# Performance work log

Measured on AMD Instinct MI355X. Metric: run time of the kernel, lower is better.

The kernel has to match this reference:

```python
import jax, jax.numpy as jnp
import numpy as np

IMG_SIZE = 640
NUM_CLASSES = 80
KA = 3
STRIDES = (8, 16, 32)
CONF_THRESH = 0.001
NMS_THRESH = 0.6
ANCHORS = np.array([[12, 16], [19, 36], [40, 28],
                    [36, 75], [76, 55], [72, 146],
                    [142, 110], [192, 243], [459, 401]], np.float32).reshape(3, 3, 2)
CLS_OFFSET = 4.0  # > max normalized coord (1.0); separates classes for class-wise NMS


def _make_grid(stride):
    f = IMG_SIZE // stride
    gy, gx = jnp.meshgrid(jnp.arange(f), jnp.arange(f), indexing='ij')
    # [HW, 1, 2] in (x, y) order, row-major over (H, W) like permute(1,2,0).view(-1,...)
    return jnp.stack([gx, gy], axis=-1).reshape(-1, 1, 2).astype(jnp.float32)


def _decode_level(pred, level):
    # pred: [KA*(1+C+4), H, W] -> obj [HW*KA,1], cls [HW*KA,C], boxes [HW*KA,4]
    C = NUM_CLASSES
    p = jnp.transpose(pred, (1, 2, 0)).reshape(-1, KA * (1 + C + 4))  # [HW, ch]
    obj = p[:, :KA].reshape(-1, 1)
    cls = p[:, KA:KA * (1 + C)].reshape(-1, C)
    reg = p[:, KA * (1 + C):].reshape(-1, KA, 4)
    grid = _make_grid(STRIDES[level])               # [HW, 1, 2]
    anchors = jnp.asarray(ANCHORS[level])           # [KA, 2]
    xy = (jax.nn.sigmoid(reg[..., :2]) + grid) * STRIDES[level]
    wh = jnp.exp(reg[..., 2:]) * anchors
    box = jnp.concatenate([xy - wh * 0.5, xy + wh * 0.5], axis=-1).reshape(-1, 4)
    return obj, cls, box


def _greedy_nms(boxes, scores, valid, thresh):
    # Faithful sequential greedy NMS (same math as the numpy loop), via lax.scan.
    N = boxes.shape[0]
    order = jnp.argsort(-scores)
    b = boxes[order]
    v = valid[order]
    areas = (b[:, 2] - b[:, 0]) * (b[:, 3] - b[:, 1])
    idx = jnp.arange(N)

    def step(suppressed, i):
        keep_i = v[i] & jnp.logical_not(suppressed[i])
        xx1 = jnp.maximum(b[i, 0], b[:, 0])
        yy1 = jnp.maximum(b[i, 1], b[:, 1])
        xx2 = jnp.minimum(b[i, 2], b[:, 2])
        yy2 = jnp.minimum(b[i, 3], b[:, 3])
        w = jnp.maximum(1e-28, xx2 - xx1)
        h = jnp.maximum(1e-28, yy2 - yy1)
        inter = w * h
        ovr = inter / (areas[i] + areas - inter + 1e-14)
        suppressed = suppressed | (keep_i & (ovr > thresh) & (idx > i))
        return suppressed, keep_i

    _, kept_sorted = jax.lax.scan(step, jnp.zeros(N, bool), idx)
    return jnp.zeros(N, bool).at[order].set(kept_sorted)


def _forward(pred_s, pred_m, pred_l):
    outs = [_decode_level(p, i) for i, p in enumerate((pred_s, pred_m, pred_l))]
    obj = jnp.concatenate([o[0] for o in outs], axis=0)   # [N, 1]
    cls = jnp.concatenate([o[1] for o in outs], axis=0)   # [N, C]
    box = jnp.concatenate([o[2] for o in outs], axis=0)   # [N, 4]
    bboxes = jnp.clip(box / IMG_SIZE, 0.0, 1.0)
    scores = jax.nn.sigmoid(obj) * jax.nn.softmax(cls, axis=-1)  # [N, C]
    cls_inds = jnp.argmax(scores, axis=1)
    conf = jnp.max(scores, axis=1)
    valid = conf >= CONF_THRESH
    # per-class NMS == class-offset trick: different classes never overlap
    nms_boxes = bboxes + cls_inds.astype(bboxes.dtype)[:, None] * CLS_OFFSET
    keep = _greedy_nms(jax.lax.stop_gradient(nms_boxes),
                       jax.lax.stop_gradient(conf), valid, NMS_THRESH)
    return bboxes, conf, cls_inds, keep


def setup_inputs() -> dict:
    key = jax.random.key(0)
    k1, k2, k3 = jax.random.split(key, 3)
    ch = KA * (1 + NUM_CLASSES + 4)  # 255
    return {
        'pred_s': jax.random.normal(k1, (ch, 80, 80), jnp.float32),
        'pred_m': jax.random.normal(k2, (ch, 40, 40), jnp.float32),
        'pred_l': jax.random.normal(k3, (ch, 20, 20), jnp.float32),
    }


def reference(pred_s, pred_m, pred_l):
    # returns fixed-shape (bboxes [N,4], scores [N], cls_inds [N], keep mask [N])
    return _forward(pred_s, pred_m, pred_l)
```

## Files before the change

### kernel.cpp

```cpp
#include <hip/hip_runtime.h>

typedef unsigned long long u64;
typedef unsigned int u32;

#define N_TOT 25200
#define NCLS 80
#define CAP 512

__device__ __constant__ float c_AW[9] = {12.f,19.f,40.f,36.f,76.f,72.f,142.f,192.f,459.f};
__device__ __constant__ float c_AH[9] = {16.f,36.f,28.f,75.f,55.f,146.f,110.f,243.f,401.f};

__global__ __launch_bounds__(256)
void decode_kernel(const float* __restrict__ p0,
                   const float* __restrict__ p1,
                   const float* __restrict__ p2,
                   float* __restrict__ out)
{
    const int t = blockIdx.x * 256 + threadIdx.x;
    const int n = t >> 3;
    const int q = t & 7;
    if (n >= N_TOT) return;

    const float* p; int f, strd, base, lvl;
    if (n < 19200)      { p = p0; f = 80; strd = 8;  base = 0;     lvl = 0; }
    else if (n < 24000) { p = p1; f = 40; strd = 16; base = 19200; lvl = 1; }
    else                { p = p2; f = 20; strd = 32; base = 24000; lvl = 2; }

    const int r  = n - base;
    const int hw = r / 3;
    const int a  = r - hw * 3;
    const int HW = f * f;
    const int gx = hw % f;
    const int gy = hw / f;
    const float* cell = p + hw;
    const float* clsp = cell + (3 + a * NCLS) * HW;

    float obj = 0.f, tx = 0.f, ty = 0.f, tw = 0.f, th = 0.f;
    if (q == 0) {
        obj = cell[a * HW];
        const float* regp = cell + (243 + a * 4) * HW;
        tx = regp[0];
        ty = regp[HW];
        tw = regp[2 * HW];
        th = regp[3 * HW];
    }

    float v[10];
    #pragma unroll
    for (int k = 0; k < 10; ++k) v[k] = clsp[(8 * k + q) * HW];

    float lmax = v[0];
    #pragma unroll
    for (int k = 1; k < 10; ++k) lmax = fmaxf(lmax, v[k]);
    float gm = lmax;
    gm = fmaxf(gm, __shfl_xor(gm, 1));
    gm = fmaxf(gm, __shfl_xor(gm, 2));
    gm = fmaxf(gm, __shfl_xor(gm, 4));

    float ls = 0.f, bp = -1.f; int ba_ = 0;
    #pragma unroll
    for (int k = 0; k < 10; ++k) {
        float pc = expf(v[k] - gm);
        ls += pc;
        if (pc > bp) { bp = pc; ba_ = 8 * k + q; }
    }
    float gs = ls;
    gs += __shfl_xor(gs, 1);
    gs += __shfl_xor(gs, 2);
    gs += __shfl_xor(gs, 4);
    {
        float bp2; int ba2;
        bp2 = __shfl_xor(bp, 1); ba2 = __shfl_xor(ba_, 1);
        if (bp2 > bp || (bp2 == bp && ba2 < ba_)) { bp = bp2; ba_ = ba2; }
        bp2 = __shfl_xor(bp, 2); ba2 = __shfl_xor(ba_, 2);
        if (bp2 > bp || (bp2 == bp && ba2 < ba_)) { bp = bp2; ba_ = ba2; }
        bp2 = __shfl_xor(bp, 4); ba2 = __shfl_xor(ba_, 4);
        if (bp2 > bp || (bp2 == bp && ba2 < ba_)) { bp = bp2; ba_ = ba2; }
    }

    if (q != 0) return;

    float sig  = 1.f / (1.f + expf(-obj));
    float conf = sig * (bp / gs);

    float sx = 1.f / (1.f + expf(-tx));
    float sy = 1.f / (1.f + expf(-ty));
    float cx = (sx + (float)gx) * (float)strd;
    float cy = (sy + (float)gy) * (float)strd;
    const int ai = lvl * 3 + a;
    float w  = expf(tw) * c_AW[ai];
    float h  = expf(th) * c_AH[ai];
    float hx = w * 0.5f, hy = h * 0.5f;
    float x1 = (cx - hx) / 640.0f;
    float y1 = (cy - hy) / 640.0f;
    float x2 = (cx + hx) / 640.0f;
    float y2 = (cy + hy) / 640.0f;
    x1 = fminf(fmaxf(x1, 0.f), 1.f);
    y1 = fminf(fmaxf(y1, 0.f), 1.f);
    x2 = fminf(fmaxf(x2, 0.f), 1.f);
    y2 = fminf(fmaxf(y2, 0.f), 1.f);

    *(float4*)(out + n * 4) = make_float4(x1, y1, x2, y2);
    out[100800 + n] = conf;
    out[126000 + n] = (float)ba_;
    out[151200 + n] = 0.0f;
}

__global__ __launch_bounds__(1024)
void nms_kernel(const float* __restrict__ out,
                float* __restrict__ out_keep)
{
    const int c = blockIdx.x;
    const int tid = threadIdx.x;
    const int wave = tid >> 6, lane = tid & 63;

    __shared__ int    scnt;
    __shared__ u64    skey[CAP];
    __shared__ float4 sbox[CAP + 1];
    __shared__ int    sgi[CAP];
    __shared__ u64    maskT[8 * CAP];

    if (tid == 0) scnt = 0;
    __syncthreads();

    const float* confp = out + 100800;
    const float* clsp  = out + 126000;
    const u64 lt = (1ull << lane) - 1ull;
    for (int itr = 0; itr < 7; ++itr) {
        const int ib = itr * 1024 + tid;
        const bool inb = (ib < 6300);
        float4 cf4 = make_float4(-1.f, -1.f, -1.f, -1.f);
        float4 cl4 = make_float4(0.f, 0.f, 0.f, 0.f);
        if (inb) {
            cf4 = *(const float4*)(confp + ib * 4);
            cl4 = *(const float4*)(clsp  + ib * 4);
        }
        const bool m0 = inb && ((int)cl4.x == c) && (cf4.x >= 0.001f);
        const bool m1 = inb && ((int)cl4.y == c) && (cf4.y >= 0.001f);
        const bool m2 = inb && ((int)cl4.z == c) && (cf4.z >= 0.001f);
        const bool m3 = inb && ((int)cl4.w == c) && (cf4.w >= 0.001f);
        const u64 b0 = __ballot(m0), b1 = __ballot(m1), b2 = __ballot(m2), b3 = __ballot(m3);
        const int t0 = __popcll(b0), t1 = __popcll(b1), t2 = __popcll(b2), t3 = __popcll(b3);
        const int tot = t0 + t1 + t2 + t3;
        int base = 0;
        if (tot) {
            if (lane == 0) base = atomicAdd(&scnt, tot);
            base = __shfl(base, 0);
            const int i0 = itr * 4096 + tid * 4;
            int pos;
            if (m0) { pos = base + __popcll(b0 & lt);
                      if (pos < CAP) skey[pos] = ((u64)__float_as_uint(cf4.x) << 32) | (u64)(~(u32)(i0)); }
            if (m1) { pos = base + t0 + __popcll(b1 & lt);
                      if (pos < CAP) skey[pos] = ((u64)__float_as_uint(cf4.y) << 32) | (u64)(~(u32)(i0 + 1)); }
            if (m2) { pos = base + t0 + t1 + __popcll(b2 & lt);
                      if (pos < CAP) skey[pos] = ((u64)__float_as_uint(cf4.z) << 32) | (u64)(~(u32)(i0 + 2)); }
            if (m3) { pos = base + t0 + t1 + t2 + __popcll(b3 & lt);
                      if (pos < CAP) skey[pos] = ((u64)__float_as_uint(cf4.w) << 32) | (u64)(~(u32)(i0 + 3)); }
        }
    }
    __syncthreads();
    const int M  = min(scnt, CAP);
    const int MW = (M + 63) >> 6;

    if (wave < MW) {
        const int e = (wave << 6) + lane;
        if (e < M) {
            const u64 ke = skey[e];
            int rank = 0;
            int j = 0;
            for (; j + 8 <= M; j += 8) {
                rank += (int)(skey[j]   > ke) + (int)(skey[j+1] > ke)
                      + (int)(skey[j+2] > ke) + (int)(skey[j+3] > ke)
                      + (int)(skey[j+4] > ke) + (int)(skey[j+5] > ke)
                      + (int)(skey[j+6] > ke) + (int)(skey[j+7] > ke);
            }
            for (; j < M; ++j) rank += (int)(skey[j] > ke);

            const u32 gi = ~(u32)ke;
            const float4 b = *(const float4*)(out + gi * 4);
            const float off = 4.0f * (float)c;
            sbox[rank] = make_float4(b.x + off, b.y + off, b.z + off, b.w + off);
            sgi[rank]  = (int)gi;
        }
    }
    __syncthreads();

    const int ntiles = (MW * (MW + 1)) >> 1;
    for (int t = wave; t < ntiles; t += 16) {
        int rw = 0, acc = 0;
        while (t >= acc + (MW - rw)) { acc += MW - rw; ++rw; }
        const int cw = rw + (t - acc);
        const int j  = (cw << 6) + lane;
        const float4 cb = sbox[min(j, M - 1)];
        const float  ca = (cb.z - cb.x) * (cb.w - cb.y);
        const int r0 = rw << 6;
        const int r1 = min(r0 + 64, M);
        u64 bits = 0ull;
        float4 nb = sbox[r0];
        for (int i = r0; i < r1; ++i) {
            const float4 rb = nb;
            nb = sbox[i + 1];
            const float ra = (rb.z - rb.x) * (rb.w - rb.y);
            float xx1 = fmaxf(rb.x, cb.x);
            float yy1 = fmaxf(rb.y, cb.y);
            float xx2 = fminf(rb.z, cb.z);
            float yy2 = fminf(rb.w, cb.w);
            float ww = fmaxf(1e-28f, xx2 - xx1);
            float hh = fmaxf(1e-28f, yy2 - yy1);
            float inter = ww * hh;
            float ovr = inter / (ra + ca - inter + 1e-14f);
            bits |= (u64)((i < j) && (ovr >= 0.6f)) << (i & 63);
        }
        maskT[rw * CAP + j] = bits;
    }
    __syncthreads();

    if (wave != 0) return;

    u64 k0 = 0, k1 = 0, k2 = 0, k3 = 0, k4 = 0, k5 = 0, k6 = 0, k7 = 0;
    (void)k7;
#define MT(W) maskT[(W) * CAP + j]
#define TILE(W, PRE)                                                    \
    if ((W) < MW) {                                                     \
        const int j = ((W) << 6) + lane;                                \
        const u64 mine = MT(W);                                         \
        const u64 pre = (PRE);                                          \
        const int rm = M - ((W) << 6);                                  \
        const u64 valid = (rm >= 64) ? ~0ull : ((1ull << rm) - 1ull);   \
        u64 cand = valid & ~__ballot(pre != 0ull);                      \
        u64 kept = 0ull;                                                \
        while (cand) {                                                  \
            const u64 remv = cand & __ballot((mine & kept) != 0ull);    \
            cand &= ~remv;                                              \
            const u64 newk = cand & __ballot((mine & cand) == 0ull);    \
            kept |= newk;                                               \
            cand &= ~newk;                                              \
        }                                                               \
        k##W = kept;                                                    \
        if ((kept >> lane) & 1ull) out_keep[sgi[j]] = 1.0f;             \
    }
    TILE(0, 0ull)
    TILE(1, (MT(0)&k0))
    TILE(2, (MT(0)&k0)|(MT(1)&k1))
    TILE(3, (MT(0)&k0)|(MT(1)&k1)|(MT(2)&k2))
    TILE(4, (MT(0)&k0)|(MT(1)&k1)|(MT(2)&k2)|(MT(3)&k3))
    TILE(5, (MT(0)&k0)|(MT(1)&k1)|(MT(2)&k2)|(MT(3)&k3)|(MT(4)&k4))
    TILE(6, (MT(0)&k0)|(MT(1)&k1)|(MT(2)&k2)|(MT(3)&k3)|(MT(4)&k4)|(MT(5)&k5))
    TILE(7, (MT(0)&k0)|(MT(1)&k1)|(MT(2)&k2)|(MT(3)&k3)|(MT(4)&k4)|(MT(5)&k5)|(MT(6)&k6))
#undef TILE
#undef MT
}

extern "C" void kernel_launch(void* const* d_in, const int* in_sizes, int n_in,
                              void* d_out, int out_size, void* d_ws, size_t ws_size,
                              hipStream_t stream) {
    const float* p0 = (const float*)d_in[0];
    const float* p1 = (const float*)d_in[1];
    const float* p2 = (const float*)d_in[2];
    float* out = (float*)d_out;

    decode_kernel<<<(N_TOT * 8 + 255) / 256, 256, 0, stream>>>(p0, p1, p2, out);
    nms_kernel<<<NCLS, 1024, 0, stream>>>(out, out + 151200);
}
```

Measured before the change: 47.16 us.

## Use 4 threads per anchor in decode and unroll NMS loads and IoU loops

```diff
diff --git a/kernel.cpp b/kernel.cpp
--- a/kernel.cpp
+++ b/kernel.cpp
@@ -17,8 +17,8 @@
                    float* __restrict__ out)
 {
     const int t = blockIdx.x * 256 + threadIdx.x;
-    const int n = t >> 3;
-    const int q = t & 7;
+    const int n = t >> 2;
+    const int q = t & 3;
     if (n >= N_TOT) return;
 
     const float* p; int f, strd, base, lvl;
@@ -34,49 +34,46 @@
     const int gy = hw / f;
     const float* cell = p + hw;
     const float* clsp = cell + (3 + a * NCLS) * HW;
-
-    float obj = 0.f, tx = 0.f, ty = 0.f, tw = 0.f, th = 0.f;
-    if (q == 0) {
-        obj = cell[a * HW];
-        const float* regp = cell + (243 + a * 4) * HW;
-        tx = regp[0];
-        ty = regp[HW];
-        tw = regp[2 * HW];
-        th = regp[3 * HW];
-    }
-
-    float v[10];
-    #pragma unroll
-    for (int k = 0; k < 10; ++k) v[k] = clsp[(8 * k + q) * HW];
+    const float* regp = cell + (243 + a * 4) * HW;
+
+    const float rv  = regp[q * HW];
+    const float obj = cell[a * HW];
+
+    float v[20];
+    #pragma unroll
+    for (int k = 0; k < 20; ++k) v[k] = clsp[(4 * k + q) * HW];
 
     float lmax = v[0];
     #pragma unroll
-    for (int k = 1; k < 10; ++k) lmax = fmaxf(lmax, v[k]);
+    for (int k = 1; k < 20; ++k) lmax = fmaxf(lmax, v[k]);
     float gm = lmax;
     gm = fmaxf(gm, __shfl_xor(gm, 1));
     gm = fmaxf(gm, __shfl_xor(gm, 2));
-    gm = fmaxf(gm, __shfl_xor(gm, 4));
 
     float ls = 0.f, bp = -1.f; int ba_ = 0;
     #pragma unroll
-    for (int k = 0; k < 10; ++k) {
+    for (int k = 0; k < 20; ++k) {
         float pc = expf(v[k] - gm);
         ls += pc;
-        if (pc > bp) { bp = pc; ba_ = 8 * k + q; }
+        if (pc > bp) { bp = pc; ba_ = 4 * k + q; }
     }
     float gs = ls;
     gs += __shfl_xor(gs, 1);
     gs += __shfl_xor(gs, 2);
-    gs += __shfl_xor(gs, 4);
     {
         float bp2; int ba2;
         bp2 = __shfl_xor(bp, 1); ba2 = __shfl_xor(ba_, 1);
         if (bp2 > bp || (bp2 == bp && ba2 < ba_)) { bp = bp2; ba_ = ba2; }
         bp2 = __shfl_xor(bp, 2); ba2 = __shfl_xor(ba_, 2);
         if (bp2 > bp || (bp2 == bp && ba2 < ba_)) { bp = bp2; ba_ = ba2; }
-        bp2 = __shfl_xor(bp, 4); ba2 = __shfl_xor(ba_, 4);
-        if (bp2 > bp || (bp2 == bp && ba2 < ba_)) { bp = bp2; ba_ = ba2; }
-    }
+    }
+
+    const int lane = threadIdx.x & 63;
+    const int gb = lane & 60;
+    const float tx = __shfl(rv, gb);
+    const float ty = __shfl(rv, gb + 1);
+    const float tw = __shfl(rv, gb + 2);
+    const float th = __shfl(rv, gb + 3);
 
     if (q != 0) return;
 
@@ -125,37 +122,44 @@
 
     const float* confp = out + 100800;
     const float* clsp  = out + 126000;
-    const u64 lt = (1ull << lane) - 1ull;
+    float4 cf[7], cl[7];
+    bool   inb[7];
+    #pragma unroll
     for (int itr = 0; itr < 7; ++itr) {
         const int ib = itr * 1024 + tid;
-        const bool inb = (ib < 6300);
-        float4 cf4 = make_float4(-1.f, -1.f, -1.f, -1.f);
-        float4 cl4 = make_float4(0.f, 0.f, 0.f, 0.f);
-        if (inb) {
-            cf4 = *(const float4*)(confp + ib * 4);
-            cl4 = *(const float4*)(clsp  + ib * 4);
-        }
-        const bool m0 = inb && ((int)cl4.x == c) && (cf4.x >= 0.001f);
-        const bool m1 = inb && ((int)cl4.y == c) && (cf4.y >= 0.001f);
-        const bool m2 = inb && ((int)cl4.z == c) && (cf4.z >= 0.001f);
-        const bool m3 = inb && ((int)cl4.w == c) && (cf4.w >= 0.001f);
+        inb[itr] = (ib < 6300);
+        if (inb[itr]) {
+            cf[itr] = *(const float4*)(confp + ib * 4);
+            cl[itr] = *(const float4*)(clsp  + ib * 4);
+        } else {
+            cf[itr] = make_float4(-1.f, -1.f, -1.f, -1.f);
+            cl[itr] = make_float4(0.f, 0.f, 0.f, 0.f);
+        }
+    }
+    const u64 lt = (1ull << lane) - 1ull;
+    #pragma unroll
+    for (int itr = 0; itr < 7; ++itr) {
+        const bool m0 = inb[itr] && ((int)cl[itr].x == c) && (cf[itr].x >= 0.001f);
+        const bool m1 = inb[itr] && ((int)cl[itr].y == c) && (cf[itr].y >= 0.001f);
+        const bool m2 = inb[itr] && ((int)cl[itr].z == c) && (cf[itr].z >= 0.001f);
+        const bool m3 = inb[itr] && ((int)cl[itr].w == c) && (cf[itr].w >= 0.001f);
         const u64 b0 = __ballot(m0), b1 = __ballot(m1), b2 = __ballot(m2), b3 = __ballot(m3);
         const int t0 = __popcll(b0), t1 = __popcll(b1), t2 = __popcll(b2), t3 = __popcll(b3);
         const int tot = t0 + t1 + t2 + t3;
-        int base = 0;
         if (tot) {
-            if (lane == 0) base = atomicAdd(&scnt, tot);
-            base = __shfl(base, 0);
+            int bs = 0;
+            if (lane == 0) bs = atomicAdd(&scnt, tot);
+            bs = __shfl(bs, 0);
             const int i0 = itr * 4096 + tid * 4;
             int pos;
-            if (m0) { pos = base + __popcll(b0 & lt);
-                      if (pos < CAP) skey[pos] = ((u64)__float_as_uint(cf4.x) << 32) | (u64)(~(u32)(i0)); }
-            if (m1) { pos = base + t0 + __popcll(b1 & lt);
-                      if (pos < CAP) skey[pos] = ((u64)__float_as_uint(cf4.y) << 32) | (u64)(~(u32)(i0 + 1)); }
-            if (m2) { pos = base + t0 + t1 + __popcll(b2 & lt);
-                      if (pos < CAP) skey[pos] = ((u64)__float_as_uint(cf4.z) << 32) | (u64)(~(u32)(i0 + 2)); }
-            if (m3) { pos = base + t0 + t1 + t2 + __popcll(b3 & lt);
-                      if (pos < CAP) skey[pos] = ((u64)__float_as_uint(cf4.w) << 32) | (u64)(~(u32)(i0 + 3)); }
+            if (m0) { pos = bs + __popcll(b0 & lt);
+                      if (pos < CAP) skey[pos] = ((u64)__float_as_uint(cf[itr].x) << 32) | (u64)(~(u32)(i0)); }
+            if (m1) { pos = bs + t0 + __popcll(b1 & lt);
+                      if (pos < CAP) skey[pos] = ((u64)__float_as_uint(cf[itr].y) << 32) | (u64)(~(u32)(i0 + 1)); }
+            if (m2) { pos = bs + t0 + t1 + __popcll(b2 & lt);
+                      if (pos < CAP) skey[pos] = ((u64)__float_as_uint(cf[itr].z) << 32) | (u64)(~(u32)(i0 + 2)); }
+            if (m3) { pos = bs + t0 + t1 + t2 + __popcll(b3 & lt);
+                      if (pos < CAP) skey[pos] = ((u64)__float_as_uint(cf[itr].w) << 32) | (u64)(~(u32)(i0 + 3)); }
         }
     }
     __syncthreads();
@@ -168,11 +172,15 @@
             const u64 ke = skey[e];
             int rank = 0;
             int j = 0;
-            for (; j + 8 <= M; j += 8) {
-                rank += (int)(skey[j]   > ke) + (int)(skey[j+1] > ke)
-                      + (int)(skey[j+2] > ke) + (int)(skey[j+3] > ke)
-                      + (int)(skey[j+4] > ke) + (int)(skey[j+5] > ke)
-                      + (int)(skey[j+6] > ke) + (int)(skey[j+7] > ke);
+            for (; j + 16 <= M; j += 16) {
+                rank += (int)(skey[j]    > ke) + (int)(skey[j+1]  > ke)
+                      + (int)(skey[j+2]  > ke) + (int)(skey[j+3]  > ke)
+                      + (int)(skey[j+4]  > ke) + (int)(skey[j+5]  > ke)
+                      + (int)(skey[j+6]  > ke) + (int)(skey[j+7]  > ke)
+                      + (int)(skey[j+8]  > ke) + (int)(skey[j+9]  > ke)
+                      + (int)(skey[j+10] > ke) + (int)(skey[j+11] > ke)
+                      + (int)(skey[j+12] > ke) + (int)(skey[j+13] > ke)
+                      + (int)(skey[j+14] > ke) + (int)(skey[j+15] > ke);
             }
             for (; j < M; ++j) rank += (int)(skey[j] > ke);
 
@@ -185,34 +193,44 @@
     }
     __syncthreads();
 
+#define IOU_BIT(RB, I) {                                                \
+        const float ra = ((RB).z - (RB).x) * ((RB).w - (RB).y);         \
+        float xx1 = fmaxf((RB).x, cb.x);                                \
+        float yy1 = fmaxf((RB).y, cb.y);                                \
+        float xx2 = fminf((RB).z, cb.z);                                \
+        float yy2 = fminf((RB).w, cb.w);                                \
+        float ww = fmaxf(1e-28f, xx2 - xx1);                            \
+        float hh = fmaxf(1e-28f, yy2 - yy1);                            \
+        float inter = ww * hh;                                          \
+        float ovr = inter / (ra + ca - inter + 1e-14f);                 \
+        bits |= (u64)(((I) < j) && (ovr >= 0.6f)) << ((I) & 63);        \
+    }
     const int ntiles = (MW * (MW + 1)) >> 1;
-    for (int t = wave; t < ntiles; t += 16) {
+    for (int tt = wave; tt < ntiles; tt += 16) {
         int rw = 0, acc = 0;
-        while (t >= acc + (MW - rw)) { acc += MW - rw; ++rw; }
-        const int cw = rw + (t - acc);
+        while (tt >= acc + (MW - rw)) { acc += MW - rw; ++rw; }
+        const int cw = rw + (tt - acc);
         const int j  = (cw << 6) + lane;
         const float4 cb = sbox[min(j, M - 1)];
         const float  ca = (cb.z - cb.x) * (cb.w - cb.y);
         const int r0 = rw << 6;
         const int r1 = min(r0 + 64, M);
         u64 bits = 0ull;
-        float4 nb = sbox[r0];
-        for (int i = r0; i < r1; ++i) {
-            const float4 rb = nb;
-            nb = sbox[i + 1];
-            const float ra = (rb.z - rb.x) * (rb.w - rb.y);
-            float xx1 = fmaxf(rb.x, cb.x);
-            float yy1 = fmaxf(rb.y, cb.y);
-            float xx2 = fminf(rb.z, cb.z);
-            float yy2 = fminf(rb.w, cb.w);
-            float ww = fmaxf(1e-28f, xx2 - xx1);
-            float hh = fmaxf(1e-28f, yy2 - yy1);
-            float inter = ww * hh;
-            float ovr = inter / (ra + ca - inter + 1e-14f);
-            bits |= (u64)((i < j) && (ovr >= 0.6f)) << (i & 63);
+        int i = r0;
+        for (; i + 4 <= r1; i += 4) {
+            const float4 b0 = sbox[i];
+            const float4 b1 = sbox[i + 1];
+            const float4 b2 = sbox[i + 2];
+            const float4 b3 = sbox[i + 3];
+            IOU_BIT(b0, i) IOU_BIT(b1, i + 1) IOU_BIT(b2, i + 2) IOU_BIT(b3, i + 3)
+        }
+        for (; i < r1; ++i) {
+            const float4 b0 = sbox[i];
+            IOU_BIT(b0, i)
         }
         maskT[rw * CAP + j] = bits;
     }
+#undef IOU_BIT
     __syncthreads();
 
     if (wave != 0) return;
@@ -259,6 +277,6 @@
     const float* p2 = (const float*)d_in[2];
     float* out = (float*)d_out;
 
-    decode_kernel<<<(N_TOT * 8 + 255) / 256, 256, 0, stream>>>(p0, p1, p2, out);
+    decode_kernel<<<(N_TOT * 4 + 255) / 256, 256, 0, stream>>>(p0, p1, p2, out);
     nms_kernel<<<NCLS, 1024, 0, stream>>>(out, out + 151200);
 }
```

Result: faster. 43.85 us (-7.0%).
